# Kernel tuning notes

Hardware: AMD Instinct MI355X
Metric: run time of the kernel (lower is better)

## Reference

```python
import jax, jax.numpy as jnp
import numpy as np

B, D_IN, D_H = 8192, 1024, 1024


def setup_inputs() -> dict:
    key = jax.random.key(0)
    ks = jax.random.split(key, 11)
    s_in = 1.0 / np.sqrt(D_IN)
    s_h = 1.0 / np.sqrt(D_H)
    return {
        "x": jax.random.normal(ks[0], (B, D_IN), jnp.float32),
        "h": jax.random.normal(ks[1], (B, D_H), jnp.float32),
        "Wiz": jax.random.normal(ks[2], (D_IN, D_H), jnp.float32) * s_in,
        "Uhz": jax.random.normal(ks[3], (D_H, D_H), jnp.float32) * s_h,
        "bz": jax.random.normal(ks[4], (D_H,), jnp.float32) * 0.01,
        "Wir": jax.random.normal(ks[5], (D_IN, D_H), jnp.float32) * s_in,
        "Uhr": jax.random.normal(ks[6], (D_H, D_H), jnp.float32) * s_h,
        "br": jax.random.normal(ks[7], (D_H,), jnp.float32) * 0.01,
        "Win": jax.random.normal(ks[8], (D_IN, D_H), jnp.float32) * s_in,
        "Uhn": jax.random.normal(ks[9], (D_H, D_H), jnp.float32) * s_h,
        "bn": jax.random.normal(ks[10], (D_H,), jnp.float32) * 0.01,
    }


def reference(x, h, Wiz, Uhz, bz, Wir, Uhr, br, Win, Uhn, bn):
    # Concatenate input-side weights into one GEMM for efficiency; math identical.
    Wi = jnp.concatenate([Wiz, Wir, Win], axis=1)          # [D_in, 3H]
    xz, xr, xn = jnp.split(x @ Wi, 3, axis=1)              # each [B, H]
    Uh = jnp.concatenate([Uhz, Uhr], axis=1)               # [H, 2H]
    hz, hr = jnp.split(h @ Uh, 2, axis=1)
    z = jax.nn.sigmoid(xz + hz + bz)
    r = jax.nn.sigmoid(xr + hr + br)
    # Faithful to source: (r * h) @ Uhn, and act1 (sigmoid) for n, not tanh.
    n = jax.nn.sigmoid(xn + (r * h) @ Uhn + bn)
    return (1.0 - z) * h + z * n
```

## Files before the change

### kernel.cpp

```cpp
#include <hip/hip_runtime.h>
#include <hip/hip_bf16.h>

typedef __attribute__((ext_vector_type(8))) short short8;
typedef __attribute__((ext_vector_type(4))) float f32x4;

#define DEV __device__ __forceinline__

DEV float bf2f(unsigned short u) {
    union { unsigned int i; float f; } v;
    v.i = ((unsigned int)u) << 16;
    return v.f;
}
DEV unsigned short f2bf(float f) {
    union { float f; unsigned int i; } v; v.f = f;
    unsigned int r = v.i + 0x7FFFu + ((v.i >> 16) & 1u);
    return (unsigned short)(r >> 16);
}
DEV float sigmoidf_(float x) {
    return 1.0f / (1.0f + __expf(-x));
}

__global__ void conv_xh(const float* __restrict__ x, const float* __restrict__ h,
                        unsigned short* __restrict__ xw, unsigned short* __restrict__ hw,
                        int n)
{
    int i = (blockIdx.x * blockDim.x + threadIdx.x) * 8;
    const float* src; unsigned short* dst; int off;
    if (i < n) { src = x; dst = xw; off = i; }
    else       { src = h; dst = hw; off = i - n; }
    float4 a = *(const float4*)(src + off);
    float4 b = *(const float4*)(src + off + 4);
    union { uint4 v; unsigned short s[8]; } o;
    o.s[0]=f2bf(a.x); o.s[1]=f2bf(a.y); o.s[2]=f2bf(a.z); o.s[3]=f2bf(a.w);
    o.s[4]=f2bf(b.x); o.s[5]=f2bf(b.y); o.s[6]=f2bf(b.z); o.s[7]=f2bf(b.w);
    *(uint4*)(dst + off) = o.v;
}

__global__ void tconv(const float* __restrict__ Wiz, const float* __restrict__ Uhz,
                      const float* __restrict__ Wir, const float* __restrict__ Uhr,
                      const float* __restrict__ Win, const float* __restrict__ Uhn,
                      unsigned short* __restrict__ B1t, unsigned short* __restrict__ B3t)
{
    __shared__ float lds[32][33];
    const float* src; unsigned short* dst;
    switch (blockIdx.z) {
        case 0: src=Wiz; dst=B1t;                            break;
        case 1: src=Uhz; dst=B1t + 1024;                     break;
        case 2: src=Wir; dst=B1t + (size_t)1024*2048;        break;
        case 3: src=Uhr; dst=B1t + (size_t)1024*2048 + 1024; break;
        case 4: src=Win; dst=B3t;                            break;
        default: src=Uhn; dst=B3t + 1024;                    break;
    }
    int k0 = blockIdx.x * 32, n0 = blockIdx.y * 32;
    int tx = threadIdx.x & 31, ty = threadIdx.x >> 5;
    #pragma unroll
    for (int i = 0; i < 4; i++)
        lds[ty + 8*i][tx] = src[(size_t)(k0 + ty + 8*i)*1024 + n0 + tx];
    __syncthreads();
    #pragma unroll
    for (int i = 0; i < 4; i++)
        dst[(size_t)(n0 + ty + 8*i)*2048 + k0 + tx] = f2bf(lds[tx][ty + 8*i]);
}

DEV void stage_band_A(char* smem, const unsigned short* A0, const unsigned short* A1,
                      int buf, int band, int ktile, int gm, int tid)
{
    const unsigned short* src = (ktile < 16) ? A0 : A1;
    int kofs = (ktile & 15) * 64;
    #pragma unroll
    for (int j = 0; j < 2; ++j) {
        int o   = tid * 16 + j * 8192;
        int rp  = o >> 7;
        int kel = (((o >> 4) & 7) ^ (rp & 7)) << 3;
        int m   = ((rp >> 6) << 7) | (band << 6) | (rp & 63);
        const unsigned short* g = src + (size_t)(gm + m) * 1024 + kofs + kel;
        __builtin_amdgcn_global_load_lds(
            (const __attribute__((address_space(1))) void*)g,
            (__attribute__((address_space(3))) void*)(smem + buf*32768 + band*16384 + o),
            16, 0, 0);
    }
}
DEV void stage_band_B(char* smem, const unsigned short* Bt,
                      int buf, int band, int ktile, int gn, int tid)
{
    #pragma unroll
    for (int j = 0; j < 2; ++j) {
        int o   = tid * 16 + j * 8192;
        int rp  = o >> 7;
        int kel = (((o >> 4) & 7) ^ (rp & 7)) << 3;
        int n   = ((rp >> 5) << 6) | (band << 5) | (rp & 31);
        const unsigned short* g = Bt + (size_t)(gn + n) * 2048 + ktile * 64 + kel;
        __builtin_amdgcn_global_load_lds(
            (const __attribute__((address_space(1))) void*)g,
            (__attribute__((address_space(3))) void*)(smem + 65536 + buf*32768 + band*16384 + o),
            16, 0, 0);
    }
}

#define LOAD_A(BUF,MH)                                                        \
    { _Pragma("unroll") for (int mi = 0; mi < 4; mi++)                        \
      { _Pragma("unroll") for (int ks = 0; ks < 2; ks++)                      \
        af[mi][ks] = *(const short8*)(smem + (BUF)*32768 + (MH)*16384         \
                        + arow + mi*2048 + ((((ks<<2)|lk)<<4) ^ aswz)); } }
#define LOAD_B(BUF,NH,DST)                                                    \
    { _Pragma("unroll") for (int ni = 0; ni < 2; ni++)                        \
      { _Pragma("unroll") for (int ks = 0; ks < 2; ks++)                      \
        DST[ni][ks] = *(const short8*)(smem + (BUF)*32768 + (NH)*16384        \
                        + brow + ni*2048 + ((((ks<<2)|lk)<<4) ^ aswz)); } }
#define MM(MH,NH,BF)                                                          \
    { _Pragma("unroll") for (int mi = 0; mi < 4; mi++)                        \
      { _Pragma("unroll") for (int ni = 0; ni < 2; ni++)                      \
        { _Pragma("unroll") for (int ks = 0; ks < 2; ks++)                    \
          acc[(MH)*4+mi][(NH)*2+ni] = __builtin_amdgcn_mfma_f32_16x16x32_bf16(\
              af[mi][ks], BF[ni][ks], acc[(MH)*4+mi][(NH)*2+ni], 0, 0, 0); } } }
#define PH_MID(DO_VM)                                                         \
    if (DO_VM) asm volatile("s_waitcnt vmcnt(6)" ::: "memory");               \
    __builtin_amdgcn_s_barrier();                                             \
    asm volatile("s_waitcnt lgkmcnt(0)" ::: "memory");                        \
    __builtin_amdgcn_s_setprio(1);
#define PH_END                                                                \
    __builtin_amdgcn_s_setprio(0);                                            \
    __builtin_amdgcn_s_barrier();

__global__ __launch_bounds__(512, 2)
void gemm1_8ph(const unsigned short* __restrict__ A0,
               const unsigned short* __restrict__ A1,
               const unsigned short* __restrict__ Bt,
               const float* __restrict__ bz, const float* __restrict__ br,
               const float* __restrict__ hsrc,
               float* __restrict__ zbuf, unsigned short* __restrict__ rh)
{
    extern __shared__ char smem[];
    const int tid = threadIdx.x;

    const int bid = blockIdx.x;
    const int xcd = bid & 7, j = bid >> 3;
    const int mt  = (xcd >> 1) * 8 + (j >> 2);
    const int nt  = (xcd & 1) * 4 + (j & 3);
    const int gm = mt * 256, gn = nt * 256;

    const int w  = tid >> 6, l = tid & 63;
    const int wr = w >> 2, wc = w & 3;
    const int lr = l & 15, lk = l >> 4;

    const int arow = wr*8192 + lr*128;
    const int brow = 65536 + wc*4096 + lr*128;
    const int aswz = (lr & 7) << 4;

    f32x4 acc[8][4] = {};
    short8 af[4][2], bf0[2][2], bf1[2][2];

    stage_band_A(smem, A0, A1, 0, 0, 0, gm, tid);
    stage_band_A(smem, A0, A1, 0, 1, 0, gm, tid);
    stage_band_B(smem, Bt, 0, 0, 0, gn, tid);
    stage_band_B(smem, Bt, 0, 1, 0, gn, tid);
    stage_band_A(smem, A0, A1, 1, 0, 1, gm, tid);
    stage_band_B(smem, Bt, 1, 0, 1, gn, tid);
    stage_band_B(smem, Bt, 1, 1, 1, gn, tid);
    asm volatile("s_waitcnt vmcnt(6)" ::: "memory");
    __builtin_amdgcn_s_barrier();

    for (int it = 0; it < 16; ++it) {
        const int T  = 2 * it;
        const int t1 = (T+1 < 31) ? T+1 : 31;
        const int t2 = (T+2 < 31) ? T+2 : 31;
        const int t3 = (T+3 < 31) ? T+3 : 31;

        LOAD_A(0,0); LOAD_B(0,0,bf0);
        stage_band_A(smem, A0, A1, 1, 1, t1, gm, tid);
        PH_MID(false); MM(0,0,bf0); PH_END;

        LOAD_B(0,1,bf1);
        stage_band_A(smem, A0, A1, 0, 0, t2, gm, tid);
        PH_MID(false); MM(0,1,bf1); PH_END;

        LOAD_A(0,1);
        stage_band_B(smem, Bt, 0, 0, t2, gn, tid);
        PH_MID(false); MM(1,0,bf0); PH_END;

        stage_band_B(smem, Bt, 0, 1, t2, gn, tid);
        PH_MID(true); MM(1,1,bf1); PH_END;

        LOAD_A(1,0); LOAD_B(1,0,bf0);
        stage_band_A(smem, A0, A1, 0, 1, t2, gm, tid);
        PH_MID(false); MM(0,0,bf0); PH_END;

        LOAD_B(1,1,bf1);
        stage_band_A(smem, A0, A1, 1, 0, t3, gm, tid);
        PH_MID(false); MM(0,1,bf1); PH_END;

        LOAD_A(1,1);
        stage_band_B(smem, Bt, 1, 0, t3, gn, tid);
        PH_MID(false); MM(1,0,bf0); PH_END;

        stage_band_B(smem, Bt, 1, 1, t3, gn, tid);
        PH_MID(true); MM(1,1,bf1); PH_END;
    }

    #pragma unroll
    for (int Mi = 0; Mi < 8; Mi++) {
        #pragma unroll
        for (int jj = 0; jj < 4; jj++) {
            int row = gm + wr*128 + Mi*16 + lk*4 + jj;
            #pragma unroll
            for (int Ni = 0; Ni < 4; Ni++) {
                int col = gn + wc*64 + Ni*16 + lr;
                float v = acc[Mi][Ni][jj];
                if (col < 1024) {
                    zbuf[(size_t)row*1024 + col] = sigmoidf_(v + bz[col]);
                } else {
                    int c = col - 1024;
                    float rv = sigmoidf_(v + br[c]);
                    rh[(size_t)row*1024 + c] = f2bf(rv * hsrc[(size_t)row*1024 + c]);
                }
            }
        }
    }
}

__global__ __launch_bounds__(256, 2)
void gemm2_m97(const unsigned short* __restrict__ A0,
               const unsigned short* __restrict__ A1,
               const unsigned short* __restrict__ Bt,
               const float* __restrict__ bn,
               const float* __restrict__ hsrc,
               const float* __restrict__ zbuf,
               float* __restrict__ out)
{
    __shared__ unsigned short lA[128*32];
    __shared__ unsigned short lB[128*32];
    const int tid = threadIdx.x;
    const int gm = blockIdx.x * 128, gn = blockIdx.y * 128;

    const int w  = tid >> 6, l = tid & 63;
    const int wm = (w >> 1) * 64, wn = (w & 1) * 64;
    const int lr = l & 15, lk = l >> 4;

    f32x4 acc[4][4] = {};

    const int srow = tid >> 2;
    const int scol = (tid & 3) * 8;
    char* lAp = (char*)lA + tid * 16;
    char* lBp = (char*)lB + tid * 16;

    for (int kt = 0; kt < 2048; kt += 32) {
        const unsigned short* Ab = (kt < 1024 ? A0 : A1)
                                 + (size_t)(gm + srow) * 1024 + (kt & 1023) + scol;
        const unsigned short* Bb = Bt + (size_t)(gn + srow) * 2048 + kt + scol;
        __syncthreads();
        __builtin_amdgcn_global_load_lds(
            (const __attribute__((address_space(1))) void*)Ab,
            (__attribute__((address_space(3))) void*)lAp, 16, 0, 0);
        __builtin_amdgcn_global_load_lds(
            (const __attribute__((address_space(1))) void*)(Ab + (size_t)64*1024),
            (__attribute__((address_space(3))) void*)(lAp + 4096), 16, 0, 0);
        __builtin_amdgcn_global_load_lds(
            (const __attribute__((address_space(1))) void*)Bb,
            (__attribute__((address_space(3))) void*)lBp, 16, 0, 0);
        __builtin_amdgcn_global_load_lds(
            (const __attribute__((address_space(1))) void*)(Bb + (size_t)64*2048),
            (__attribute__((address_space(3))) void*)(lBp + 4096), 16, 0, 0);
        __syncthreads();

        short8 af[4], bfr[4];
        #pragma unroll
        for (int mi = 0; mi < 4; mi++)
            af[mi] = *(const short8*)&lA[(wm + mi*16 + lr)*32 + lk*8];
        #pragma unroll
        for (int ni = 0; ni < 4; ni++)
            bfr[ni] = *(const short8*)&lB[(wn + ni*16 + lr)*32 + lk*8];
        #pragma unroll
        for (int mi = 0; mi < 4; mi++)
            #pragma unroll
            for (int ni = 0; ni < 4; ni++)
                acc[mi][ni] = __builtin_amdgcn_mfma_f32_16x16x32_bf16(
                    af[mi], bfr[ni], acc[mi][ni], 0, 0, 0);
    }

    #pragma unroll
    for (int mi = 0; mi < 4; mi++) {
        #pragma unroll
        for (int j = 0; j < 4; j++) {
            int row = gm + wm + mi*16 + lk*4 + j;
            #pragma unroll
            for (int ni = 0; ni < 4; ni++) {
                int col = gn + wn + ni*16 + lr;
                float nv = sigmoidf_(acc[mi][ni][j] + bn[col]);
                float zv = zbuf[(size_t)row*1024 + col];
                float hv = hsrc[(size_t)row*1024 + col];
                out[(size_t)row*1024 + col] = (1.0f - zv)*hv + zv*nv;
            }
        }
    }
}

extern "C" void kernel_launch(void* const* d_in, const int* in_sizes, int n_in,
                              void* d_out, int out_size, void* d_ws, size_t ws_size,
                              hipStream_t stream)
{
    const float* x   = (const float*)d_in[0];
    const float* h   = (const float*)d_in[1];
    const float* Wiz = (const float*)d_in[2];
    const float* Uhz = (const float*)d_in[3];
    const float* bz  = (const float*)d_in[4];
    const float* Wir = (const float*)d_in[5];
    const float* Uhr = (const float*)d_in[6];
    const float* br  = (const float*)d_in[7];
    const float* Win = (const float*)d_in[8];
    const float* Uhn = (const float*)d_in[9];
    const float* bn  = (const float*)d_in[10];
    float* out = (float*)d_out;

    char* ws = (char*)d_ws;
    const size_t MB = 1024ull * 1024ull;
    unsigned short* xw   = (unsigned short*)(ws + 0);
    unsigned short* hw   = (unsigned short*)(ws + 16*MB);
    unsigned short* B1t  = (unsigned short*)(ws + 32*MB);
    unsigned short* B3t  = (unsigned short*)(ws + 40*MB);
    float*          zbuf = (float*)(ws + 44*MB);
    unsigned short* rh   = (unsigned short*)(ws + 76*MB);

    const int B = 8192, H = 1024;

    (void)hipFuncSetAttribute((const void*)gemm1_8ph,
                              hipFuncAttributeMaxDynamicSharedMemorySize, 131072);

    conv_xh<<<dim3(2*B*H/8/256), dim3(256), 0, stream>>>(x, h, xw, hw, B*H);

    tconv<<<dim3(32, 32, 6), dim3(256), 0, stream>>>(
        Wiz, Uhz, Wir, Uhr, Win, Uhn, B1t, B3t);

    gemm1_8ph<<<dim3(256), dim3(512), 131072, stream>>>(
        xw, hw, B1t, bz, br, h, zbuf, rh);

    gemm2_m97<<<dim3(64, 8), dim3(256), 0, stream>>>(
        xw, rh, B3t, bn, h, zbuf, out);
}
```

Before: 296.0 us.

## Interleave activations into concatenated [x|h] and [x|r*h] buffers to simplify GEMM staging

```diff
diff --git a/kernel.cpp b/kernel.cpp
--- a/kernel.cpp
+++ b/kernel.cpp
@@ -5,6 +5,8 @@
 typedef __attribute__((ext_vector_type(4))) float f32x4;
 
 #define DEV __device__ __forceinline__
+#define AS1 __attribute__((address_space(1)))
+#define AS3 __attribute__((address_space(3)))
 
 DEV float bf2f(unsigned short u) {
     union { unsigned int i; float f; } v;
@@ -21,19 +23,26 @@
 }
 
 __global__ void conv_xh(const float* __restrict__ x, const float* __restrict__ h,
-                        unsigned short* __restrict__ xw, unsigned short* __restrict__ hw,
-                        int n)
-{
-    int i = (blockIdx.x * blockDim.x + threadIdx.x) * 8;
-    const float* src; unsigned short* dst; int off;
-    if (i < n) { src = x; dst = xw; off = i; }
-    else       { src = h; dst = hw; off = i - n; }
+                        unsigned short* __restrict__ xh, unsigned short* __restrict__ xr)
+{
+    const int nX = 8192 * 1024 / 8;
+    int i = blockIdx.x * blockDim.x + threadIdx.x;
+    const float* src; int off;
+    bool isx = i < nX;
+    if (isx) { src = x; off = i * 8; }
+    else     { src = h; off = (i - nX) * 8; }
+    int row = off >> 10, col = off & 1023;
     float4 a = *(const float4*)(src + off);
     float4 b = *(const float4*)(src + off + 4);
     union { uint4 v; unsigned short s[8]; } o;
     o.s[0]=f2bf(a.x); o.s[1]=f2bf(a.y); o.s[2]=f2bf(a.z); o.s[3]=f2bf(a.w);
     o.s[4]=f2bf(b.x); o.s[5]=f2bf(b.y); o.s[6]=f2bf(b.z); o.s[7]=f2bf(b.w);
-    *(uint4*)(dst + off) = o.v;
+    if (isx) {
+        *(uint4*)(xh + (size_t)row*2048 + col) = o.v;
+        *(uint4*)(xr + (size_t)row*2048 + col) = o.v;
+    } else {
+        *(uint4*)(xh + (size_t)row*2048 + 1024 + col) = o.v;
+    }
 }
 
 __global__ void tconv(const float* __restrict__ Wiz, const float* __restrict__ Uhz,
@@ -62,40 +71,14 @@
         dst[(size_t)(n0 + ty + 8*i)*2048 + k0 + tx] = f2bf(lds[tx][ty + 8*i]);
 }
 
-DEV void stage_band_A(char* smem, const unsigned short* A0, const unsigned short* A1,
-                      int buf, int band, int ktile, int gm, int tid)
-{
-    const unsigned short* src = (ktile < 16) ? A0 : A1;
-    int kofs = (ktile & 15) * 64;
-    #pragma unroll
-    for (int j = 0; j < 2; ++j) {
-        int o   = tid * 16 + j * 8192;
-        int rp  = o >> 7;
-        int kel = (((o >> 4) & 7) ^ (rp & 7)) << 3;
-        int m   = ((rp >> 6) << 7) | (band << 6) | (rp & 63);
-        const unsigned short* g = src + (size_t)(gm + m) * 1024 + kofs + kel;
-        __builtin_amdgcn_global_load_lds(
-            (const __attribute__((address_space(1))) void*)g,
-            (__attribute__((address_space(3))) void*)(smem + buf*32768 + band*16384 + o),
-            16, 0, 0);
-    }
-}
-DEV void stage_band_B(char* smem, const unsigned short* Bt,
-                      int buf, int band, int ktile, int gn, int tid)
-{
-    #pragma unroll
-    for (int j = 0; j < 2; ++j) {
-        int o   = tid * 16 + j * 8192;
-        int rp  = o >> 7;
-        int kel = (((o >> 4) & 7) ^ (rp & 7)) << 3;
-        int n   = ((rp >> 5) << 6) | (band << 5) | (rp & 31);
-        const unsigned short* g = Bt + (size_t)(gn + n) * 2048 + ktile * 64 + kel;
-        __builtin_amdgcn_global_load_lds(
-            (const __attribute__((address_space(1))) void*)g,
-            (__attribute__((address_space(3))) void*)(smem + 65536 + buf*32768 + band*16384 + o),
-            16, 0, 0);
-    }
-}
+#define GLD(SRC,DST) __builtin_amdgcn_global_load_lds(                        \
+    (const AS1 void*)(SRC), (AS3 void*)(DST), 16, 0, 0)
+#define STAGE_A(BUF,BAND,KT)                                                  \
+    GLD(gA##BAND##0 + (size_t)(KT)*64, smA + (BUF)*32768 + (BAND)*16384);     \
+    GLD(gA##BAND##1 + (size_t)(KT)*64, smA + (BUF)*32768 + (BAND)*16384 + 8192);
+#define STAGE_B(BUF,BAND,KT)                                                  \
+    GLD(gB##BAND##0 + (size_t)(KT)*64, smB + (BUF)*32768 + (BAND)*16384);     \
+    GLD(gB##BAND##1 + (size_t)(KT)*64, smB + (BUF)*32768 + (BAND)*16384 + 8192);
 
 #define LOAD_A(BUF,MH)                                                        \
     { _Pragma("unroll") for (int mi = 0; mi < 4; mi++)                        \
@@ -108,9 +91,9 @@
         DST[ni][ks] = *(const short8*)(smem + (BUF)*32768 + (NH)*16384        \
                         + brow + ni*2048 + ((((ks<<2)|lk)<<4) ^ aswz)); } }
 #define MM(MH,NH,BF)                                                          \
-    { _Pragma("unroll") for (int mi = 0; mi < 4; mi++)                        \
-      { _Pragma("unroll") for (int ni = 0; ni < 2; ni++)                      \
-        { _Pragma("unroll") for (int ks = 0; ks < 2; ks++)                    \
+    { _Pragma("unroll") for (int ks = 0; ks < 2; ks++)                        \
+      { _Pragma("unroll") for (int mi = 0; mi < 4; mi++)                      \
+        { _Pragma("unroll") for (int ni = 0; ni < 2; ni++)                    \
           acc[(MH)*4+mi][(NH)*2+ni] = __builtin_amdgcn_mfma_f32_16x16x32_bf16(\
               af[mi][ks], BF[ni][ks], acc[(MH)*4+mi][(NH)*2+ni], 0, 0, 0); } } }
 #define PH_MID(DO_VM)                                                         \
@@ -123,12 +106,11 @@
     __builtin_amdgcn_s_barrier();
 
 __global__ __launch_bounds__(512, 2)
-void gemm1_8ph(const unsigned short* __restrict__ A0,
-               const unsigned short* __restrict__ A1,
+void gemm1_8ph(const unsigned short* __restrict__ xh,
                const unsigned short* __restrict__ Bt,
                const float* __restrict__ bz, const float* __restrict__ br,
                const float* __restrict__ hsrc,
-               float* __restrict__ zbuf, unsigned short* __restrict__ rh)
+               float* __restrict__ zbuf, unsigned short* __restrict__ xr)
 {
     extern __shared__ char smem[];
     const int tid = threadIdx.x;
@@ -147,16 +129,25 @@
     const int brow = 65536 + wc*4096 + lr*128;
     const int aswz = (lr & 7) << 4;
 
+    const int s   = tid >> 3;
+    const int kel = ((tid & 7) ^ (s & 7)) << 3;
+    char* smA = smem + tid * 16;
+    char* smB = smem + 65536 + tid * 16;
+    const unsigned short* gA00 = xh + (size_t)(gm +        s      )*2048 + kel;
+    const unsigned short* gA01 = xh + (size_t)(gm + 128 +  s      )*2048 + kel;
+    const unsigned short* gA10 = xh + (size_t)(gm +  64 +  s      )*2048 + kel;
+    const unsigned short* gA11 = xh + (size_t)(gm + 192 +  s      )*2048 + kel;
+    const int nb = ((s >> 5) << 6) | (s & 31);
+    const unsigned short* gB00 = Bt + (size_t)(gn +       nb      )*2048 + kel;
+    const unsigned short* gB01 = Bt + (size_t)(gn + 128 + nb      )*2048 + kel;
+    const unsigned short* gB10 = Bt + (size_t)(gn +  32 + nb      )*2048 + kel;
+    const unsigned short* gB11 = Bt + (size_t)(gn + 160 + nb      )*2048 + kel;
+
     f32x4 acc[8][4] = {};
     short8 af[4][2], bf0[2][2], bf1[2][2];
 
-    stage_band_A(smem, A0, A1, 0, 0, 0, gm, tid);
-    stage_band_A(smem, A0, A1, 0, 1, 0, gm, tid);
-    stage_band_B(smem, Bt, 0, 0, 0, gn, tid);
-    stage_band_B(smem, Bt, 0, 1, 0, gn, tid);
-    stage_band_A(smem, A0, A1, 1, 0, 1, gm, tid);
-    stage_band_B(smem, Bt, 1, 0, 1, gn, tid);
-    stage_band_B(smem, Bt, 1, 1, 1, gn, tid);
+    STAGE_A(0,0,0); STAGE_A(0,1,0); STAGE_B(0,0,0); STAGE_B(0,1,0);
+    STAGE_A(1,0,1); STAGE_B(1,0,1); STAGE_B(1,1,1);
     asm volatile("s_waitcnt vmcnt(6)" ::: "memory");
     __builtin_amdgcn_s_barrier();
 
@@ -167,33 +158,33 @@
         const int t3 = (T+3 < 31) ? T+3 : 31;
 
         LOAD_A(0,0); LOAD_B(0,0,bf0);
-        stage_band_A(smem, A0, A1, 1, 1, t1, gm, tid);
+        STAGE_A(1,1,t1);
         PH_MID(false); MM(0,0,bf0); PH_END;
 
         LOAD_B(0,1,bf1);
-        stage_band_A(smem, A0, A1, 0, 0, t2, gm, tid);
+        STAGE_A(0,0,t2);
         PH_MID(false); MM(0,1,bf1); PH_END;
 
         LOAD_A(0,1);
-        stage_band_B(smem, Bt, 0, 0, t2, gn, tid);
+        STAGE_B(0,0,t2);
         PH_MID(false); MM(1,0,bf0); PH_END;
 
-        stage_band_B(smem, Bt, 0, 1, t2, gn, tid);
+        STAGE_B(0,1,t2);
         PH_MID(true); MM(1,1,bf1); PH_END;
 
         LOAD_A(1,0); LOAD_B(1,0,bf0);
-        stage_band_A(smem, A0, A1, 0, 1, t2, gm, tid);
+        STAGE_A(0,1,t2);
         PH_MID(false); MM(0,0,bf0); PH_END;
 
         LOAD_B(1,1,bf1);
-        stage_band_A(smem, A0, A1, 1, 0, t3, gm, tid);
+        STAGE_A(1,0,t3);
         PH_MID(false); MM(0,1,bf1); PH_END;
 
         LOAD_A(1,1);
-        stage_band_B(smem, Bt, 1, 0, t3, gn, tid);
+        STAGE_B(1,0,t3);
         PH_MID(false); MM(1,0,bf0); PH_END;
 
-        stage_band_B(smem, Bt, 1, 1, t3, gn, tid);
+        STAGE_B(1,1,t3);
         PH_MID(true); MM(1,1,bf1); PH_END;
     }
 
@@ -211,7 +202,8 @@
                 } else {
                     int c = col - 1024;
                     float rv = sigmoidf_(v + br[c]);
-                    rh[(size_t)row*1024 + c] = f2bf(rv * hsrc[(size_t)row*1024 + c]);
+                    xr[(size_t)row*2048 + 1024 + c] =
+                        f2bf(rv * hsrc[(size_t)row*1024 + c]);
                 }
             }
         }
@@ -219,8 +211,7 @@
 }
 
 __global__ __launch_bounds__(256, 2)
-void gemm2_m97(const unsigned short* __restrict__ A0,
-               const unsigned short* __restrict__ A1,
+void gemm2_m97(const unsigned short* __restrict__ A,
                const unsigned short* __restrict__ Bt,
                const float* __restrict__ bn,
                const float* __restrict__ hsrc,
@@ -243,23 +234,15 @@
     char* lAp = (char*)lA + tid * 16;
     char* lBp = (char*)lB + tid * 16;
 
+    const unsigned short* Ab0 = A  + (size_t)(gm + srow) * 2048 + scol;
+    const unsigned short* Bb0 = Bt + (size_t)(gn + srow) * 2048 + scol;
+
     for (int kt = 0; kt < 2048; kt += 32) {
-        const unsigned short* Ab = (kt < 1024 ? A0 : A1)
-                                 + (size_t)(gm + srow) * 1024 + (kt & 1023) + scol;
-        const unsigned short* Bb = Bt + (size_t)(gn + srow) * 2048 + kt + scol;
         __syncthreads();
-        __builtin_amdgcn_global_load_lds(
-            (const __attribute__((address_space(1))) void*)Ab,
-            (__attribute__((address_space(3))) void*)lAp, 16, 0, 0);
-        __builtin_amdgcn_global_load_lds(
-            (const __attribute__((address_space(1))) void*)(Ab + (size_t)64*1024),
-            (__attribute__((address_space(3))) void*)(lAp + 4096), 16, 0, 0);
-        __builtin_amdgcn_global_load_lds(
-            (const __attribute__((address_space(1))) void*)Bb,
-            (__attribute__((address_space(3))) void*)lBp, 16, 0, 0);
-        __builtin_amdgcn_global_load_lds(
-            (const __attribute__((address_space(1))) void*)(Bb + (size_t)64*2048),
-            (__attribute__((address_space(3))) void*)(lBp + 4096), 16, 0, 0);
+        GLD(Ab0 + kt,                     lAp);
+        GLD(Ab0 + kt + (size_t)64*2048,   lAp + 4096);
+        GLD(Bb0 + kt,                     lBp);
+        GLD(Bb0 + kt + (size_t)64*2048,   lBp + 4096);
         __syncthreads();
 
         short8 af[4], bfr[4];
@@ -313,26 +296,23 @@
 
     char* ws = (char*)d_ws;
     const size_t MB = 1024ull * 1024ull;
-    unsigned short* xw   = (unsigned short*)(ws + 0);
-    unsigned short* hw   = (unsigned short*)(ws + 16*MB);
-    unsigned short* B1t  = (unsigned short*)(ws + 32*MB);
-    unsigned short* B3t  = (unsigned short*)(ws + 40*MB);
-    float*          zbuf = (float*)(ws + 44*MB);
-    unsigned short* rh   = (unsigned short*)(ws + 76*MB);
-
-    const int B = 8192, H = 1024;
+    unsigned short* xh   = (unsigned short*)(ws + 0);
+    unsigned short* xr   = (unsigned short*)(ws + 32*MB);
+    unsigned short* B1t  = (unsigned short*)(ws + 64*MB);
+    unsigned short* B3t  = (unsigned short*)(ws + 72*MB);
+    float*          zbuf = (float*)(ws + 76*MB);
 
     (void)hipFuncSetAttribute((const void*)gemm1_8ph,
                               hipFuncAttributeMaxDynamicSharedMemorySize, 131072);
 
-    conv_xh<<<dim3(2*B*H/8/256), dim3(256), 0, stream>>>(x, h, xw, hw, B*H);
+    conv_xh<<<dim3(8192), dim3(256), 0, stream>>>(x, h, xh, xr);
 
     tconv<<<dim3(32, 32, 6), dim3(256), 0, stream>>>(
         Wiz, Uhz, Wir, Uhr, Win, Uhn, B1t, B3t);
 
     gemm1_8ph<<<dim3(256), dim3(512), 131072, stream>>>(
-        xw, hw, B1t, bz, br, h, zbuf, rh);
+        xh, B1t, bz, br, h, zbuf, xr);
 
     gemm2_m97<<<dim3(64, 8), dim3(256), 0, stream>>>(
-        xw, rh, B3t, bn, h, zbuf, out);
-}
+        xr, B3t, bn, h, zbuf, out);
+}
```

After: 297.9 us. No clear change (+0.6%).
